# Kernel tuning notes

Hardware: AMD Instinct MI355X
Metric: run time of the kernel (lower is better)

The kernel has to match this reference:

```python
import jax, jax.numpy as jnp
import numpy as np

B, N, D = 8, 2048, 256
BIG = 1e9  # max_int_value used to mask the diagonal
LN_EPS = 1e-5  # F.layer_norm default eps


def setup_inputs() -> dict:
    key = jax.random.key(0)
    kq, kk = jax.random.split(key)
    q = jax.random.normal(kq, (B, N, D), dtype=jnp.float32)
    k = jax.random.normal(kk, (B, N, D), dtype=jnp.float32)
    return {"q": q, "k": k, "top_k_instances": 100, "top_k_relationships": 5}


def _forward(q, k, K, R):
    b, n, d = q.shape
    # dense QK^T + softmax over keys -> (b, n, n)
    scores1 = jax.nn.softmax(jnp.einsum('bid,bjd->bij', q, k), axis=-1)
    # instance selection: top-K of the softmaxed diagonal, sorted ascending
    diag = jnp.diagonal(scores1, axis1=-2, axis2=-1)           # (b, n)
    top_idx = jnp.sort(jax.lax.top_k(diag, K)[1], axis=-1)      # (b, K)
    # gather selected rows then selected columns -> (b, K, K)
    sel = jnp.take_along_axis(scores1, top_idx[:, :, None], axis=1)   # (b, K, n)
    rel = jnp.take_along_axis(sel, jnp.broadcast_to(top_idx[:, None, :], (b, K, K)), axis=2)
    # mask diagonal with BIG (masked_fill_ with eye)
    rel = jnp.where(jnp.eye(K, dtype=bool)[None], BIG, rel)
    # top-R relationships per selected instance; torch recovers them via
    # scatter(-1)+where, which yields row-major order with ascending column
    # indices inside each row -> equivalent to sorting top-k indices per row.
    rel_idx = jnp.sort(jax.lax.top_k(rel, R)[1], axis=-1)       # (b, K, R)
    rows = jnp.broadcast_to(jnp.arange(K)[:, None], (K, R)).reshape(-1)  # (K*R,)
    subj = top_idx[:, rows]                                     # (b, K*R) original subject ids
    obj = jnp.take_along_axis(top_idx, rel_idx.reshape(b, K * R), axis=-1)  # (b, K*R)
    batch_ids = jnp.broadcast_to(jnp.arange(b)[:, None], (b, K * R))
    soi = jnp.stack([batch_ids, subj, obj], axis=-1)            # (b, K*R, 3)
    # gather embeddings from q and layer-norm (no affine)
    se = jnp.take_along_axis(q, subj[:, :, None], axis=1)       # (b, K*R, d)
    oe = jnp.take_along_axis(q, obj[:, :, None], axis=1)
    re = se + oe
    mu = jnp.mean(re, axis=-1, keepdims=True)
    var = jnp.var(re, axis=-1, keepdims=True)
    re = (re - mu) * jax.lax.rsqrt(var + LN_EPS)
    return scores1, soi, re


def reference(q, k, top_k_instances, top_k_relationships):
    return _forward(q, k, top_k_instances, top_k_relationships)
```

## Files before the change

kernel.cpp:

```cpp
#include <hip/hip_runtime.h>
#include <math.h>

#define BB 8
#define NN 2048
#define DD 256
#define KK 100
#define RR 5
#define BIGV 1000000000.0f
#define LN_EPS 1e-5f

typedef __attribute__((ext_vector_type(8))) short short8;
typedef __attribute__((ext_vector_type(4))) float floatx4;

__device__ static inline unsigned short f2bf_rne(float x) {
  unsigned int u = __float_as_uint(x);
  unsigned int r = (u + 0x7FFFu + ((u >> 16) & 1u)) >> 16;
  return (unsigned short)r;
}
__device__ static inline float bf2f(unsigned short h) {
  return __uint_as_float(((unsigned int)h) << 16);
}

__device__ static inline void gl_lds16(const unsigned short* g, unsigned short* l) {
  __builtin_amdgcn_global_load_lds(
      (const __attribute__((address_space(1))) unsigned int*)(g),
      (__attribute__((address_space(3))) unsigned int*)(l), 16, 0, 0);
}

__global__ __launch_bounds__(256) void split_bf16(const float* __restrict__ q,
                                                  const float* __restrict__ k,
                                                  ushort4* __restrict__ qhi,
                                                  ushort4* __restrict__ qlo,
                                                  ushort4* __restrict__ khi,
                                                  ushort4* __restrict__ klo) {
  const int n4 = BB * NN * DD / 4;
  const float4* src = (blockIdx.y == 0) ? (const float4*)q : (const float4*)k;
  ushort4* hi = blockIdx.y ? khi : qhi;
  ushort4* lo = blockIdx.y ? klo : qlo;
  for (int i = blockIdx.x * 256 + threadIdx.x; i < n4; i += gridDim.x * 256) {
    float4 v = src[i];
    ushort4 h, l;
    h.x = f2bf_rne(v.x); l.x = f2bf_rne(v.x - bf2f(h.x));
    h.y = f2bf_rne(v.y); l.y = f2bf_rne(v.y - bf2f(h.y));
    h.z = f2bf_rne(v.z); l.z = f2bf_rne(v.z - bf2f(h.z));
    h.w = f2bf_rne(v.w); l.w = f2bf_rne(v.w - bf2f(h.w));
    hi[i] = h; lo[i] = l;
  }
}

__global__ __launch_bounds__(256) void gemm_mfma_split(
    const unsigned short* __restrict__ qhi, const unsigned short* __restrict__ qlo,
    const unsigned short* __restrict__ khi, const unsigned short* __restrict__ klo,
    float* __restrict__ s) {
  __shared__ unsigned short lds[2][4][8][512];

  const int lid = blockIdx.x + ((blockIdx.y + (blockIdx.z << 4)) << 4);
  const int swz = ((lid & 7) << 8) + (lid >> 3);
  const int bx = swz & 15;
  const int by = (swz >> 4) & 15;
  const int b = swz >> 8;
  const int i0 = by * 128, j0 = bx * 128;

  const int t = threadIdx.x;
  const int w = t >> 6, L = t & 63;
  const int wx = w & 1, wy = w >> 1;
  const int q_ = L >> 4, m_ = L & 15;

  const size_t bofs = (size_t)b * NN * DD;
  const unsigned short* base;
  {
    const unsigned short* b0 = qhi + bofs;
    const unsigned short* b1 = qlo + bofs;
    const unsigned short* b2 = khi + bofs;
    const unsigned short* b3 = klo + bofs;
    base = (w == 0) ? b0 : (w == 1) ? b1 : (w == 2) ? b2 : b3;
  }
  const int rowbase = (w < 2 ? i0 : j0);
  const unsigned short* gbase = base + (size_t)(rowbase + m_) * DD + q_ * 8;

  floatx4 acc[4][4];
#pragma unroll
  for (int i = 0; i < 4; ++i)
#pragma unroll
    for (int j = 0; j < 4; ++j) acc[i][j] = (floatx4){0.f, 0.f, 0.f, 0.f};

#define STAGE(buf, kb0)                                              \
  _Pragma("unroll") for (int r = 0; r < 8; ++r)                      \
      gl_lds16(gbase + (size_t)r * 16 * DD + (kb0), &lds[buf][w][r][0]);

  STAGE(0, 0);
  int cur = 0;
#pragma unroll
  for (int it = 0; it < 8; ++it) {
    if (it < 7) {
      STAGE(cur ^ 1, (it + 1) * 32);
      asm volatile("s_waitcnt vmcnt(8)" ::: "memory");
    } else {
      asm volatile("s_waitcnt vmcnt(0)" ::: "memory");
    }
    __builtin_amdgcn_s_barrier();

    short8 ah[4], al[4], bh[4], bl[4];
#pragma unroll
    for (int i = 0; i < 4; ++i) {
      ah[i] = *(const short8*)&lds[cur][0][wy * 4 + i][L * 8];
      al[i] = *(const short8*)&lds[cur][1][wy * 4 + i][L * 8];
      bh[i] = *(const short8*)&lds[cur][2][wx * 4 + i][L * 8];
      bl[i] = *(const short8*)&lds[cur][3][wx * 4 + i][L * 8];
    }
#pragma unroll
    for (int i = 0; i < 4; ++i)
#pragma unroll
      for (int j = 0; j < 4; ++j) {
        acc[i][j] = __builtin_amdgcn_mfma_f32_16x16x32_bf16(ah[i], bh[j], acc[i][j], 0, 0, 0);
        acc[i][j] = __builtin_amdgcn_mfma_f32_16x16x32_bf16(ah[i], bl[j], acc[i][j], 0, 0, 0);
        acc[i][j] = __builtin_amdgcn_mfma_f32_16x16x32_bf16(al[i], bh[j], acc[i][j], 0, 0, 0);
      }
    __builtin_amdgcn_s_barrier();
    cur ^= 1;
  }
#undef STAGE

#pragma unroll
  for (int i = 0; i < 4; ++i)
#pragma unroll
    for (int j = 0; j < 4; ++j)
#pragma unroll
      for (int r = 0; r < 4; ++r) {
        int row = i0 + wy * 64 + i * 16 + q_ * 4 + r;
        int col = j0 + wx * 64 + j * 16 + m_;
        s[((size_t)b * NN + row) * NN + col] = acc[i][j][r];
      }
}

__global__ __launch_bounds__(256) void gemm_logits(const float* __restrict__ q,
                                                   const float* __restrict__ k,
                                                   float* __restrict__ s) {
  __shared__ float As[32][132];
  __shared__ float Bs[32][132];
  const int b = blockIdx.z;
  const int i0 = blockIdx.y * 128;
  const int j0 = blockIdx.x * 128;
  const int t = threadIdx.x;
  const int tx = t & 15;
  const int ty = t >> 4;
  const float* qb = q + (size_t)b * NN * DD;
  const float* kb = k + (size_t)b * NN * DD;

  float acc[8][8];
#pragma unroll
  for (int i = 0; i < 8; ++i)
#pragma unroll
    for (int j = 0; j < 8; ++j) acc[i][j] = 0.f;

  for (int kb0 = 0; kb0 < DD; kb0 += 32) {
#pragma unroll
    for (int l = 0; l < 4; ++l) {
      int f = l * 256 + t;
      int row = f >> 3;
      int c4 = (f & 7) * 4;
      float4 va = *(const float4*)(qb + (size_t)(i0 + row) * DD + kb0 + c4);
      float4 vb = *(const float4*)(kb + (size_t)(j0 + row) * DD + kb0 + c4);
      As[c4 + 0][row] = va.x; As[c4 + 1][row] = va.y;
      As[c4 + 2][row] = va.z; As[c4 + 3][row] = va.w;
      Bs[c4 + 0][row] = vb.x; Bs[c4 + 1][row] = vb.y;
      Bs[c4 + 2][row] = vb.z; Bs[c4 + 3][row] = vb.w;
    }
    __syncthreads();
#pragma unroll
    for (int kk = 0; kk < 32; ++kk) {
      float a[8], bv[8];
      *(float4*)&a[0] = *(const float4*)&As[kk][ty * 8];
      *(float4*)&a[4] = *(const float4*)&As[kk][ty * 8 + 4];
      *(float4*)&bv[0] = *(const float4*)&Bs[kk][tx * 8];
      *(float4*)&bv[4] = *(const float4*)&Bs[kk][tx * 8 + 4];
#pragma unroll
      for (int i = 0; i < 8; ++i)
#pragma unroll
        for (int j = 0; j < 8; ++j) acc[i][j] += a[i] * bv[j];
    }
    __syncthreads();
  }

#pragma unroll
  for (int i = 0; i < 8; ++i) {
    size_t row = (size_t)(i0 + ty * 8 + i);
    float* po = s + ((size_t)b * NN + row) * NN + j0 + tx * 8;
    *(float4*)po = make_float4(acc[i][0], acc[i][1], acc[i][2], acc[i][3]);
    *(float4*)(po + 4) = make_float4(acc[i][4], acc[i][5], acc[i][6], acc[i][7]);
  }
}

__device__ inline float pick4(float4 v, int j) {
  return j == 0 ? v.x : (j == 1 ? v.y : (j == 2 ? v.z : v.w));
}

__global__ __launch_bounds__(256) void softmax_rows(float* __restrict__ s,
                                                    float* __restrict__ diag) {
  const int bi = blockIdx.x;
  const int irow = bi & (NN - 1);
  const int t = threadIdx.x;
  float4* rowp = (float4*)(s + (size_t)bi * NN);
  float4 v0 = rowp[t];
  float4 v1 = rowp[256 + t];

  __shared__ float red[4];
  float m = fmaxf(fmaxf(fmaxf(v0.x, v0.y), fmaxf(v0.z, v0.w)),
                  fmaxf(fmaxf(v1.x, v1.y), fmaxf(v1.z, v1.w)));
#pragma unroll
  for (int off = 32; off; off >>= 1) m = fmaxf(m, __shfl_xor(m, off));
  if ((t & 63) == 0) red[t >> 6] = m;
  __syncthreads();
  m = fmaxf(fmaxf(red[0], red[1]), fmaxf(red[2], red[3]));
  __syncthreads();

  float4 e0, e1;
  e0.x = expf(v0.x - m); e0.y = expf(v0.y - m);
  e0.z = expf(v0.z - m); e0.w = expf(v0.w - m);
  e1.x = expf(v1.x - m); e1.y = expf(v1.y - m);
  e1.z = expf(v1.z - m); e1.w = expf(v1.w - m);
  float sum = e0.x + e0.y + e0.z + e0.w + e1.x + e1.y + e1.z + e1.w;
#pragma unroll
  for (int off = 32; off; off >>= 1) sum += __shfl_xor(sum, off);
  if ((t & 63) == 0) red[t >> 6] = sum;
  __syncthreads();
  sum = red[0] + red[1] + red[2] + red[3];

  float inv = 1.0f / sum;
  float4 s0 = make_float4(e0.x * inv, e0.y * inv, e0.z * inv, e0.w * inv);
  float4 s1 = make_float4(e1.x * inv, e1.y * inv, e1.z * inv, e1.w * inv);
  rowp[t] = s0;
  rowp[256 + t] = s1;

  int c0 = t * 4;
  if (irow >= c0 && irow < c0 + 4) diag[bi] = pick4(s0, irow - c0);
  int c1 = 1024 + t * 4;
  if (irow >= c1 && irow < c1 + 4) diag[bi] = pick4(s1, irow - c1);
}

__global__ __launch_bounds__(256) void topk_rank(const float* __restrict__ diag,
                                                 unsigned char* __restrict__ flags) {
  const int b = blockIdx.y;
  const int c = blockIdx.x;
  const int t = threadIdx.x;
  __shared__ unsigned long long key[NN];
  __shared__ unsigned short partial[256];

#pragma unroll
  for (int sIt = 0; sIt < 8; ++sIt) {
    int i = t + sIt * 256;
    unsigned int vb = __float_as_uint(diag[b * NN + i]);
    key[i] = ((unsigned long long)vb << 32) | (unsigned int)(NN - 1 - i);
  }
  __syncthreads();

  const int e = c * 128 + (t & 127);
  const int base = (t >> 7) * 1024;
  const unsigned long long my = key[e];
  int r = 0;
#pragma unroll 8
  for (int j = 0; j < 1024; ++j) r += (key[base + j] > my) ? 1 : 0;
  partial[t] = (unsigned short)r;
  __syncthreads();

  if (t < 128) {
    int rank = (int)partial[t] + (int)partial[t + 128];
    flags[b * NN + e] = (rank < KK) ? 1 : 0;
  }
}

__global__ __launch_bounds__(1024) void topk_compact(const unsigned char* __restrict__ flags,
                                                     int* __restrict__ topidx) {
  const int b = blockIdx.x;
  const int t = threadIdx.x;
  __shared__ unsigned long long mask[32];
  const bool f0 = flags[b * NN + t] != 0;
  const bool f1 = flags[b * NN + t + 1024] != 0;
  const unsigned long long m0 = __ballot(f0);
  const unsigned long long m1 = __ballot(f1);
  const int w = t >> 6, l = t & 63;
  if (l == 0) { mask[w] = m0; mask[16 + w] = m1; }
  __syncthreads();
  if (f0) {
    int pos = __popcll(m0 & ((1ull << l) - 1ull));
    for (int j = 0; j < w; ++j) pos += __popcll(mask[j]);
    topidx[b * KK + pos] = t;
  }
  if (f1) {
    int pos = __popcll(m1 & ((1ull << l) - 1ull));
    for (int j = 0; j < 16 + w; ++j) pos += __popcll(mask[j]);
    topidx[b * KK + pos] = t + 1024;
  }
}

__global__ __launch_bounds__(64) void rel_topk(const float* __restrict__ s,
                                               const int* __restrict__ topidx,
                                               float* __restrict__ soi,
                                               int2* __restrict__ pairs) {
  const int b = blockIdx.y;
  const int i = blockIdx.x;
  const int l = threadIdx.x;
  const int* tixb = topidx + b * KK;
  const int subj = tixb[i];
  const float* srow = s + ((size_t)b * NN + subj) * NN;

  const int j0 = l, j1 = l + 64;
  int c0 = tixb[j0];
  float v0 = (j0 == i) ? BIGV : srow[c0];
  unsigned long long k0 =
      ((unsigned long long)__float_as_uint(v0) << 32) | (unsigned int)(KK - 1 - j0);
  unsigned long long k1 = 0ull;
  if (j1 < KK) {
    int c1 = tixb[j1];
    float v1 = (j1 == i) ? BIGV : srow[c1];
    k1 = ((unsigned long long)__float_as_uint(v1) << 32) | (unsigned int)(KK - 1 - j1);
  }

  int sel[RR];
#pragma unroll
  for (int r = 0; r < RR; ++r) {
    unsigned long long best = k0 > k1 ? k0 : k1;
#pragma unroll
    for (int off = 32; off; off >>= 1) {
      unsigned long long o = __shfl_xor(best, off);
      if (o > best) best = o;
    }
    int js = KK - 1 - (int)(unsigned int)(best & 0xFFFFFFFFull);
    sel[r] = js;
    if (j0 == js) k0 = 0ull;
    if (j1 == js) k1 = 0ull;
  }

  if (l == 0) {
#pragma unroll
    for (int a2 = 0; a2 < RR; ++a2)
#pragma unroll
      for (int b2 = a2 + 1; b2 < RR; ++b2)
        if (sel[b2] < sel[a2]) { int tmp = sel[a2]; sel[a2] = sel[b2]; sel[b2] = tmp; }
#pragma unroll
    for (int r = 0; r < RR; ++r) {
      int obj = tixb[sel[r]];
      size_t p = ((size_t)b * KK + i) * RR + r;
      soi[p * 3 + 0] = (float)b;
      soi[p * 3 + 1] = (float)subj;
      soi[p * 3 + 2] = (float)obj;
      pairs[p] = make_int2(subj, obj);
    }
  }
}

__global__ __launch_bounds__(64) void edge_ln(const float* __restrict__ q,
                                              const int2* __restrict__ pairs,
                                              float* __restrict__ re) {
  const int p = blockIdx.x;
  const int b = p / (KK * RR);
  const int l = threadIdx.x;
  int2 pr = pairs[p];
  const float4* qs = (const float4*)(q + ((size_t)b * NN + pr.x) * DD);
  const float4* qo = (const float4*)(q + ((size_t)b * NN + pr.y) * DD);
  float4 a = qs[l];
  float4 o = qo[l];
  a.x += o.x; a.y += o.y; a.z += o.z; a.w += o.w;
  float sum = a.x + a.y + a.z + a.w;
  float sq = a.x * a.x + a.y * a.y + a.z * a.z + a.w * a.w;
#pragma unroll
  for (int off = 32; off; off >>= 1) {
    sum += __shfl_xor(sum, off);
    sq += __shfl_xor(sq, off);
  }
  float mu = sum * (1.f / DD);
  float var = sq * (1.f / DD) - mu * mu;
  float rs = rsqrtf(var + LN_EPS);
  float4 r4 = make_float4((a.x - mu) * rs, (a.y - mu) * rs,
                          (a.z - mu) * rs, (a.w - mu) * rs);
  ((float4*)(re + (size_t)p * DD))[l] = r4;
}

extern "C" void kernel_launch(void* const* d_in, const int* in_sizes, int n_in,
                              void* d_out, int out_size, void* d_ws, size_t ws_size,
                              hipStream_t stream) {
  const float* q = (const float*)d_in[0];
  const float* k = (const float*)d_in[1];

  float* out = (float*)d_out;
  float* scores = out;
  float* soi = out + (size_t)BB * NN * NN;
  float* re = soi + (size_t)BB * KK * RR * 3;

  char* ws = (char*)d_ws;
  float* diag = (float*)ws;
  int* topidx = (int*)(ws + (size_t)BB * NN * 4);
  int2* pairs = (int2*)(ws + (size_t)BB * NN * 4 + (size_t)BB * KK * 4);
  unsigned char* flags =
      (unsigned char*)(ws + (size_t)BB * NN * 4 + (size_t)BB * KK * 4 +
                       (size_t)BB * KK * RR * 8);
  const size_t small_end = 128 * 1024;
  const size_t plane = (size_t)BB * NN * DD * 2;
  const bool use_mfma = ws_size >= small_end + 4 * plane;

  if (use_mfma) {
    unsigned short* qhi = (unsigned short*)(ws + small_end);
    unsigned short* qlo = (unsigned short*)(ws + small_end + plane);
    unsigned short* khi = (unsigned short*)(ws + small_end + 2 * plane);
    unsigned short* klo = (unsigned short*)(ws + small_end + 3 * plane);
    split_bf16<<<dim3(1024, 2), 256, 0, stream>>>(q, k, (ushort4*)qhi, (ushort4*)qlo,
                                                  (ushort4*)khi, (ushort4*)klo);
    gemm_mfma_split<<<dim3(NN / 128, NN / 128, BB), 256, 0, stream>>>(qhi, qlo, khi, klo,
                                                                      scores);
  } else {
    gemm_logits<<<dim3(NN / 128, NN / 128, BB), 256, 0, stream>>>(q, k, scores);
  }
  softmax_rows<<<dim3(BB * NN), 256, 0, stream>>>(scores, diag);
  topk_rank<<<dim3(16, BB), 256, 0, stream>>>(diag, flags);
  topk_compact<<<dim3(BB), 1024, 0, stream>>>(flags, topidx);
  rel_topk<<<dim3(KK, BB), 64, 0, stream>>>(scores, topidx, soi, pairs);
  edge_ln<<<dim3(BB * KK * RR), 64, 0, stream>>>(q, pairs, re);
}
```

Measured before the change: 281.1 us.

## Enlarge MFMA GEMM tile to 256x128 with 8 waves and triple-buffered LDS

The split-bf16 QK^T GEMM block now uses 512 threads and computes a 256x128 output tile, so the K tile is loaded once for twice as many Q rows. The LDS pipeline goes from double to triple buffering, with the vmcnt waits adjusted to match. s_setprio is raised around the MFMA section. The goal is less redundant global traffic and better latency hiding, at the cost of more LDS per block (about 144KB) and possibly lower occupancy.

```diff
diff --git a/kernel.cpp b/kernel.cpp
--- a/kernel.cpp
+++ b/kernel.cpp
@@ -48,18 +48,18 @@
   }
 }
 
-__global__ __launch_bounds__(256) void gemm_mfma_split(
+__global__ __launch_bounds__(512, 2) void gemm_mfma_split(
     const unsigned short* __restrict__ qhi, const unsigned short* __restrict__ qlo,
     const unsigned short* __restrict__ khi, const unsigned short* __restrict__ klo,
     float* __restrict__ s) {
-  __shared__ unsigned short lds[2][4][8][512];
-
-  const int lid = blockIdx.x + ((blockIdx.y + (blockIdx.z << 4)) << 4);
-  const int swz = ((lid & 7) << 8) + (lid >> 3);
+  __shared__ unsigned short lds[3][48][512];
+
+  const int lid = blockIdx.x + ((blockIdx.y + (blockIdx.z << 3)) << 4);
+  const int swz = ((lid & 7) << 7) + (lid >> 3);
   const int bx = swz & 15;
-  const int by = (swz >> 4) & 15;
-  const int b = swz >> 8;
-  const int i0 = by * 128, j0 = bx * 128;
+  const int by = (swz >> 4) & 7;
+  const int b = swz >> 7;
+  const int i0 = by * 256, j0 = bx * 128;
 
   const int t = threadIdx.x;
   const int w = t >> 6, L = t & 63;
@@ -67,16 +67,37 @@
   const int q_ = L >> 4, m_ = L & 15;
 
   const size_t bofs = (size_t)b * NN * DD;
-  const unsigned short* base;
-  {
-    const unsigned short* b0 = qhi + bofs;
-    const unsigned short* b1 = qlo + bofs;
-    const unsigned short* b2 = khi + bofs;
-    const unsigned short* b3 = klo + bofs;
-    base = (w == 0) ? b0 : (w == 1) ? b1 : (w == 2) ? b2 : b3;
-  }
-  const int rowbase = (w < 2 ? i0 : j0);
-  const unsigned short* gbase = base + (size_t)(rowbase + m_) * DD + q_ * 8;
+
+  const unsigned short* gp0;
+  const unsigned short* gp1;
+  const unsigned short* gp2;
+  const unsigned short* gp3;
+  const unsigned short* gp4;
+  const unsigned short* gp5;
+#define MKPTR(u, dst)                                                        \
+  {                                                                          \
+    int f = w * 6 + (u);                                                     \
+    const unsigned short* pl;                                                \
+    int row;                                                                 \
+    if (f < 16) { pl = qhi; row = i0 + f * 16; }                             \
+    else if (f < 32) { pl = qlo; row = i0 + (f - 16) * 16; }                 \
+    else if (f < 40) { pl = khi; row = j0 + (f - 32) * 16; }                 \
+    else { pl = klo; row = j0 + (f - 40) * 16; }                             \
+    dst = pl + bofs + (size_t)(row + m_) * DD + q_ * 8;                      \
+  }
+  MKPTR(0, gp0) MKPTR(1, gp1) MKPTR(2, gp2)
+  MKPTR(3, gp3) MKPTR(4, gp4) MKPTR(5, gp5)
+#undef MKPTR
+
+#define STAGE(buf, kt)                                       \
+  do {                                                       \
+    gl_lds16(gp0 + (kt) * 32, &lds[buf][w * 6 + 0][0]);      \
+    gl_lds16(gp1 + (kt) * 32, &lds[buf][w * 6 + 1][0]);      \
+    gl_lds16(gp2 + (kt) * 32, &lds[buf][w * 6 + 2][0]);      \
+    gl_lds16(gp3 + (kt) * 32, &lds[buf][w * 6 + 3][0]);      \
+    gl_lds16(gp4 + (kt) * 32, &lds[buf][w * 6 + 4][0]);      \
+    gl_lds16(gp5 + (kt) * 32, &lds[buf][w * 6 + 5][0]);      \
+  } while (0)
 
   floatx4 acc[4][4];
 #pragma unroll
@@ -84,17 +105,17 @@
 #pragma unroll
     for (int j = 0; j < 4; ++j) acc[i][j] = (floatx4){0.f, 0.f, 0.f, 0.f};
 
-#define STAGE(buf, kb0)                                              \
-  _Pragma("unroll") for (int r = 0; r < 8; ++r)                      \
-      gl_lds16(gbase + (size_t)r * 16 * DD + (kb0), &lds[buf][w][r][0]);
-
   STAGE(0, 0);
-  int cur = 0;
+  STAGE(1, 1);
+
 #pragma unroll
   for (int it = 0; it < 8; ++it) {
-    if (it < 7) {
-      STAGE(cur ^ 1, (it + 1) * 32);
-      asm volatile("s_waitcnt vmcnt(8)" ::: "memory");
+    const int cur = it % 3;
+    if (it < 6) {
+      STAGE((it + 2) % 3, it + 2);
+      asm volatile("s_waitcnt vmcnt(12)" ::: "memory");
+    } else if (it == 6) {
+      asm volatile("s_waitcnt vmcnt(6)" ::: "memory");
     } else {
       asm volatile("s_waitcnt vmcnt(0)" ::: "memory");
     }
@@ -102,12 +123,17 @@
 
     short8 ah[4], al[4], bh[4], bl[4];
 #pragma unroll
+    for (int j = 0; j < 4; ++j) {
+      bh[j] = *(const short8*)&lds[cur][32 + wx * 4 + j][L * 8];
+      bl[j] = *(const short8*)&lds[cur][40 + wx * 4 + j][L * 8];
+    }
+#pragma unroll
     for (int i = 0; i < 4; ++i) {
-      ah[i] = *(const short8*)&lds[cur][0][wy * 4 + i][L * 8];
-      al[i] = *(const short8*)&lds[cur][1][wy * 4 + i][L * 8];
-      bh[i] = *(const short8*)&lds[cur][2][wx * 4 + i][L * 8];
-      bl[i] = *(const short8*)&lds[cur][3][wx * 4 + i][L * 8];
-    }
+      ah[i] = *(const short8*)&lds[cur][wy * 4 + i][L * 8];
+      al[i] = *(const short8*)&lds[cur][16 + wy * 4 + i][L * 8];
+    }
+
+    __builtin_amdgcn_s_setprio(1);
 #pragma unroll
     for (int i = 0; i < 4; ++i)
 #pragma unroll
@@ -116,8 +142,8 @@
         acc[i][j] = __builtin_amdgcn_mfma_f32_16x16x32_bf16(ah[i], bl[j], acc[i][j], 0, 0, 0);
         acc[i][j] = __builtin_amdgcn_mfma_f32_16x16x32_bf16(al[i], bh[j], acc[i][j], 0, 0, 0);
       }
+    __builtin_amdgcn_s_setprio(0);
     __builtin_amdgcn_s_barrier();
-    cur ^= 1;
   }
 #undef STAGE
 
@@ -405,7 +431,7 @@
     unsigned short* klo = (unsigned short*)(ws + small_end + 3 * plane);
     split_bf16<<<dim3(1024, 2), 256, 0, stream>>>(q, k, (ushort4*)qhi, (ushort4*)qlo,
                                                   (ushort4*)khi, (ushort4*)klo);
-    gemm_mfma_split<<<dim3(NN / 128, NN / 128, BB), 256, 0, stream>>>(qhi, qlo, khi, klo,
+    gemm_mfma_split<<<dim3(NN / 128, NN / 256, BB), 512, 0, stream>>>(qhi, qlo, khi, klo,
                                                                       scores);
   } else {
     gemm_logits<<<dim3(NN / 128, NN / 128, BB), 256, 0, stream>>>(q, k, scores);
```

After: 285.3 us. Within noise of the previous version (+1.5%).

## Load A operand directly to registers and stage only B in LDS

Applied to the files above, without the earlier changes.

The split-bf16 GEMM now reads the Q hi/lo fragments directly from global memory into registers per wave, and only the K hi/lo tiles are staged through LDS with async loads. This halves LDS use, and launch bounds now request three blocks per CU for more occupancy. s_setprio is raised around the MFMA block. The risk is redundant global reads of A across waves that share rows, and uncoalesced direct loads.

```diff
diff --git a/kernel.cpp b/kernel.cpp
--- a/kernel.cpp
+++ b/kernel.cpp
@@ -48,11 +48,11 @@
   }
 }
 
-__global__ __launch_bounds__(256) void gemm_mfma_split(
+__global__ __launch_bounds__(256, 3) void gemm_mfma_split(
     const unsigned short* __restrict__ qhi, const unsigned short* __restrict__ qlo,
     const unsigned short* __restrict__ khi, const unsigned short* __restrict__ klo,
     float* __restrict__ s) {
-  __shared__ unsigned short lds[2][4][8][512];
+  __shared__ unsigned short lds[2][2][8][512];
 
   const int lid = blockIdx.x + ((blockIdx.y + (blockIdx.z << 4)) << 4);
   const int swz = ((lid & 7) << 8) + (lid >> 3);
@@ -67,47 +67,65 @@
   const int q_ = L >> 4, m_ = L & 15;
 
   const size_t bofs = (size_t)b * NN * DD;
-  const unsigned short* base;
-  {
-    const unsigned short* b0 = qhi + bofs;
-    const unsigned short* b1 = qlo + bofs;
-    const unsigned short* b2 = khi + bofs;
-    const unsigned short* b3 = klo + bofs;
-    base = (w == 0) ? b0 : (w == 1) ? b1 : (w == 2) ? b2 : b3;
-  }
-  const int rowbase = (w < 2 ? i0 : j0);
-  const unsigned short* gbase = base + (size_t)(rowbase + m_) * DD + q_ * 8;
+
+  const unsigned short* gah = qhi + bofs + (size_t)(i0 + wy * 64 + m_) * DD + q_ * 8;
+  const unsigned short* gal = qlo + bofs + (size_t)(i0 + wy * 64 + m_) * DD + q_ * 8;
+
+  const unsigned short* gb0;
+  const unsigned short* gb1;
+  const unsigned short* gb2;
+  const unsigned short* gb3;
+#define MKB(u, dst)                                                          \
+  {                                                                          \
+    int f = w * 4 + (u);                                                     \
+    const unsigned short* pl = (f < 8) ? khi : klo;                          \
+    int ft = f & 7;                                                          \
+    dst = pl + bofs + (size_t)(j0 + ft * 16 + m_) * DD + q_ * 8;             \
+  }
+  MKB(0, gb0) MKB(1, gb1) MKB(2, gb2) MKB(3, gb3)
+#undef MKB
+
+#define STAGE(buf, kb0)                                                      \
+  do {                                                                       \
+    gl_lds16(gb0 + (kb0), &lds[buf][(w * 4 + 0) >> 3][(w * 4 + 0) & 7][0]);  \
+    gl_lds16(gb1 + (kb0), &lds[buf][(w * 4 + 1) >> 3][(w * 4 + 1) & 7][0]);  \
+    gl_lds16(gb2 + (kb0), &lds[buf][(w * 4 + 2) >> 3][(w * 4 + 2) & 7][0]);  \
+    gl_lds16(gb3 + (kb0), &lds[buf][(w * 4 + 3) >> 3][(w * 4 + 3) & 7][0]);  \
+  } while (0)
 
   floatx4 acc[4][4];
 #pragma unroll
   for (int i = 0; i < 4; ++i)
 #pragma unroll
     for (int j = 0; j < 4; ++j) acc[i][j] = (floatx4){0.f, 0.f, 0.f, 0.f};
-
-#define STAGE(buf, kb0)                                              \
-  _Pragma("unroll") for (int r = 0; r < 8; ++r)                      \
-      gl_lds16(gbase + (size_t)r * 16 * DD + (kb0), &lds[buf][w][r][0]);
 
   STAGE(0, 0);
   int cur = 0;
 #pragma unroll
   for (int it = 0; it < 8; ++it) {
+    const int kb0 = it * 32;
+    short8 ah[4], al[4];
+#pragma unroll
+    for (int i = 0; i < 4; ++i) {
+      ah[i] = *(const short8*)(gah + (size_t)i * 16 * DD + kb0);
+      al[i] = *(const short8*)(gal + (size_t)i * 16 * DD + kb0);
+    }
+    asm volatile("" ::: "memory");
     if (it < 7) {
-      STAGE(cur ^ 1, (it + 1) * 32);
-      asm volatile("s_waitcnt vmcnt(8)" ::: "memory");
+      STAGE(cur ^ 1, kb0 + 32);
+      asm volatile("s_waitcnt vmcnt(4)" ::: "memory");
     } else {
       asm volatile("s_waitcnt vmcnt(0)" ::: "memory");
     }
     __builtin_amdgcn_s_barrier();
 
-    short8 ah[4], al[4], bh[4], bl[4];
-#pragma unroll
-    for (int i = 0; i < 4; ++i) {
-      ah[i] = *(const short8*)&lds[cur][0][wy * 4 + i][L * 8];
-      al[i] = *(const short8*)&lds[cur][1][wy * 4 + i][L * 8];
-      bh[i] = *(const short8*)&lds[cur][2][wx * 4 + i][L * 8];
-      bl[i] = *(const short8*)&lds[cur][3][wx * 4 + i][L * 8];
-    }
+    short8 bh[4], bl[4];
+#pragma unroll
+    for (int j = 0; j < 4; ++j) {
+      bh[j] = *(const short8*)&lds[cur][0][wx * 4 + j][L * 8];
+      bl[j] = *(const short8*)&lds[cur][1][wx * 4 + j][L * 8];
+    }
+    __builtin_amdgcn_s_setprio(1);
 #pragma unroll
     for (int i = 0; i < 4; ++i)
 #pragma unroll
@@ -116,6 +134,7 @@
         acc[i][j] = __builtin_amdgcn_mfma_f32_16x16x32_bf16(ah[i], bl[j], acc[i][j], 0, 0, 0);
         acc[i][j] = __builtin_amdgcn_mfma_f32_16x16x32_bf16(al[i], bh[j], acc[i][j], 0, 0, 0);
       }
+    __builtin_amdgcn_s_setprio(0);
     __builtin_amdgcn_s_barrier();
     cur ^= 1;
   }
```

Measured after the change: 311.5 us. 1.11x slower.
